# Kernel optimization log

Hardware: AMD Instinct MI355X
Metric: run time of the kernel (lower is better)

## Reference

```python
import jax, jax.numpy as jnp
import numpy as np

B, S, D, H = 2, 2048, 1024, 16
HD = D // H  # head_dim = 64
ROPE_BASE = 10000.0


def _rope_cos_sin(seq_len, head_dim, dtype):
    inv_freq = 1.0 / (ROPE_BASE ** (jnp.arange(0, head_dim, 2, dtype=jnp.float32) / head_dim))
    t = jnp.arange(seq_len, dtype=jnp.float32)
    freqs = jnp.einsum('i,j->ij', t, inv_freq)            # [S, HD/2]
    emb = jnp.concatenate([freqs, freqs], axis=-1)        # [S, HD]
    return jnp.cos(emb).astype(dtype), jnp.sin(emb).astype(dtype)


def _rotate_half(x):
    x1, x2 = jnp.split(x, 2, axis=-1)
    return jnp.concatenate([-x2, x1], axis=-1)


def setup_inputs() -> dict:
    key = jax.random.key(0)
    ks = jax.random.split(key, 5)
    scale = 1.0 / np.sqrt(D)
    x = jax.random.normal(ks[0], (B, S, D), dtype=jnp.float32)
    wq = jax.random.normal(ks[1], (D, D), dtype=jnp.float32) * scale
    wk = jax.random.normal(ks[2], (D, D), dtype=jnp.float32) * scale
    wv = jax.random.normal(ks[3], (D, D), dtype=jnp.float32) * scale
    wo = jax.random.normal(ks[4], (D, D), dtype=jnp.float32) * scale
    # causal additive mask: 0 on/below diagonal, -1e9 above
    causal = jnp.triu(jnp.full((S, S), -1e9, dtype=jnp.float32), k=1)
    attention_mask = causal[None, None, :, :]
    return {'x': x, 'attention_mask': attention_mask, 'wq': wq, 'wk': wk, 'wv': wv, 'wo': wo}


def reference(x, attention_mask, wq, wk, wv, wo):
    b, s, d = x.shape
    scale = 1.0 / np.sqrt(HD)
    # projections (torch Linear: y = x @ W.T)
    q = (x @ wq.T).reshape(b, s, H, HD).transpose(0, 2, 1, 3)  # [B,H,S,HD]
    k = (x @ wk.T).reshape(b, s, H, HD).transpose(0, 2, 1, 3)
    v = (x @ wv.T).reshape(b, s, H, HD).transpose(0, 2, 1, 3)
    cos, sin = _rope_cos_sin(s, HD, x.dtype)                   # [S, HD]
    cos = cos[None, None]
    sin = sin[None, None]
    q = q * cos + _rotate_half(q) * sin
    k = k * cos + _rotate_half(k) * sin
    scores = jnp.einsum('bhqd,bhkd->bhqk', q, k) * scale       # [B,H,S,S]
    scores = scores + attention_mask
    probs = jax.nn.softmax(scores, axis=-1)
    out = jnp.einsum('bhqk,bhkd->bhqd', probs, v)              # [B,H,S,HD]
    out = out.transpose(0, 2, 1, 3).reshape(b, s, d)
    return out @ wo.T
```

## Files before the change

kernel.cpp:

```cpp
#include <hip/hip_runtime.h>
#include <cstdint>
#include <cstddef>

typedef __attribute__((ext_vector_type(8))) _Float16 half8;
typedef __attribute__((ext_vector_type(4))) _Float16 half4;
typedef __attribute__((ext_vector_type(2))) __fp16 fp16x2;
typedef __attribute__((ext_vector_type(4))) float f32x4;

#define NB 2
#define NS 2048
#define ND 1024
#define NH 16
#define NHD 64
#define NM (NB * NS)

__device__ __forceinline__ void cvt8(const float* __restrict__ s,
                                     _Float16* __restrict__ d, int g) {
  const float4* s4 = (const float4*)s + (size_t)g * 2;
  float4 a = s4[0], b = s4[1];
  half8 h;
  h[0] = (_Float16)a.x; h[1] = (_Float16)a.y;
  h[2] = (_Float16)a.z; h[3] = (_Float16)a.w;
  h[4] = (_Float16)b.x; h[5] = (_Float16)b.y;
  h[6] = (_Float16)b.z; h[7] = (_Float16)b.w;
  *(half8*)(d + (size_t)g * 8) = h;
}

__global__ void prep(const float* __restrict__ x,
                     const float* __restrict__ wq, const float* __restrict__ wk,
                     const float* __restrict__ wv, const float* __restrict__ wo,
                     _Float16* __restrict__ xb,
                     _Float16* __restrict__ wqb, _Float16* __restrict__ wkb,
                     _Float16* __restrict__ wvb, _Float16* __restrict__ wob,
                     float* __restrict__ cosT, float* __restrict__ sinT) {
  int i = blockIdx.x * 256 + threadIdx.x;
  if (i < 524288) {
    cvt8(x, xb, i);
  } else if (i < 1048576) {
    int j = i - 524288;
    int k = j >> 17, g = j & 131071;
    const float* ws = (k == 0) ? wq : (k == 1) ? wk : (k == 2) ? wv : wo;
    _Float16* wd = (k == 0) ? wqb : (k == 1) ? wkb : (k == 2) ? wvb : wob;
    cvt8(ws, wd, g);
  } else if (i < 1056768) {
    int t0 = (i - 1048576) * 8;
#pragma unroll
    for (int e = 0; e < 8; ++e) {
      int t = t0 + e;
      int s = t >> 5, j = t & 31;
      float inv = expf(-(float)(2 * j) * (9.210340371976184f / 64.0f));
      float ang = (float)s * inv;
      cosT[t] = cosf(ang);
      sinT[t] = sinf(ang);
    }
  }
}

__device__ __forceinline__ void gload_lds16(const void* g, void* lds) {
  __builtin_amdgcn_global_load_lds(
      (const __attribute__((address_space(1))) unsigned int*)g,
      (__attribute__((address_space(3))) unsigned int*)lds, 16, 0, 0);
}

__device__ __forceinline__ float exp2_fast(float x) {
  float r;
  asm("v_exp_f32 %0, %1" : "=v"(r) : "v"(x));
  return r;
}

__device__ __forceinline__ void gemm_mainloop64(const _Float16* __restrict__ A,
                                                const _Float16* __restrict__ Bw,
                                                _Float16* As, _Float16* Bs,
                                                int brow, int bcol,
                                                int lane, int wid, int tid,
                                                f32x4 acc[4][4]) {
  const int l15 = lane & 15, l4 = lane >> 4;
  const int wr = wid >> 1, wc = wid & 1;
  const int rswz = (l15 & 7) << 4;
  const int srb = tid >> 3;
  const int scb = (tid & 7) * 16;

  for (int kt = 0; kt < ND / 64; ++kt) {
    const int k0 = kt * 64;
#pragma unroll
    for (int c = 0; c < 4; ++c) {
      const int r = c * 32 + srb;
      const int sb = scb ^ ((r & 7) << 4);
      gload_lds16((const char*)(A + (size_t)(brow + r) * ND + k0) + sb,
                  (char*)As + c * 4096 + tid * 16);
      gload_lds16((const char*)(Bw + (size_t)(bcol + r) * ND + k0) + sb,
                  (char*)Bs + c * 4096 + tid * 16);
    }
    __syncthreads();
#pragma unroll
    for (int kk = 0; kk < 2; ++kk) {
      half8 af[4], bf[4];
#pragma unroll
      for (int m = 0; m < 4; ++m) {
        const int row = wr * 64 + m * 16 + l15;
        af[m] = *(const half8*)((const char*)As +
                 ((row * 128 + kk * 64 + l4 * 16) ^ rswz));
      }
#pragma unroll
      for (int n = 0; n < 4; ++n) {
        const int row = wc * 64 + n * 16 + l15;
        bf[n] = *(const half8*)((const char*)Bs +
                 ((row * 128 + kk * 64 + l4 * 16) ^ rswz));
      }
#pragma unroll
      for (int m = 0; m < 4; ++m)
#pragma unroll
        for (int n = 0; n < 4; ++n)
          acc[m][n] = __builtin_amdgcn_mfma_f32_16x16x32_f16(af[m], bf[n],
                                                             acc[m][n], 0, 0, 0);
    }
    __syncthreads();
  }
}

__launch_bounds__(256, 2)
__global__ void qkv_gemm(const _Float16* __restrict__ X,
                         const _Float16* __restrict__ Wq,
                         const _Float16* __restrict__ Wk,
                         const _Float16* __restrict__ Wv,
                         _Float16* __restrict__ Qb,
                         _Float16* __restrict__ Kb,
                         _Float16* __restrict__ Vt,
                         const float* __restrict__ cosT,
                         const float* __restrict__ sinT) {
  __shared__ __align__(16) _Float16 As[128 * 64];
  __shared__ __align__(16) _Float16 Bs[128 * 64];
  const int tid = threadIdx.x, lane = tid & 63, wid = tid >> 6;
  const int l15 = lane & 15, l4 = lane >> 4;
  const int wr = wid >> 1, wc = wid & 1;
  const int brow = blockIdx.y * 128, bcol = blockIdx.x * 128;
  const int mode = blockIdx.z;
  const _Float16* W = (mode == 0) ? Wq : (mode == 1 ? Wk : Wv);

  f32x4 acc[4][4] = {};
  gemm_mainloop64(X, W, As, Bs, brow, bcol, lane, wid, tid, acc);

  const int b = brow >> 11;
  const int sbase = (brow & (NS - 1)) + wr * 64;
  const int h = (bcol >> 6) + wc;

  if (mode < 2) {
    _Float16* oh = ((mode == 0) ? Qb : Kb) + (size_t)(b * NH + h) * NS * NHD;
#pragma unroll
    for (int m = 0; m < 4; ++m) {
#pragma unroll
      for (int r = 0; r < 4; ++r) {
        const int s = sbase + m * 16 + l4 * 4 + r;
#pragma unroll
        for (int n = 0; n < 2; ++n) {
          const int hd = n * 16 + l15;
          const float c = cosT[s * 32 + hd];
          const float sn = sinT[s * 32 + hd];
          const float lo = acc[m][n][r], hi = acc[m][n + 2][r];
          oh[(size_t)s * NHD + hd]      = (_Float16)(lo * c - hi * sn);
          oh[(size_t)s * NHD + hd + 32] = (_Float16)(hi * c + lo * sn);
        }
      }
    }
  } else {
#pragma unroll
    for (int m = 0; m < 4; ++m) {
      const int s0 = sbase + m * 16 + l4 * 4;
      const int npos = (s0 & ~63) + (m >> 1) * 32 + l4 * 8 + (m & 1) * 4;
#pragma unroll
      for (int n = 0; n < 4; ++n) {
        const int hd = n * 16 + l15;
        half4 pk;
        pk[0] = (_Float16)acc[m][n][0];
        pk[1] = (_Float16)acc[m][n][1];
        pk[2] = (_Float16)acc[m][n][2];
        pk[3] = (_Float16)acc[m][n][3];
        *(half4*)(Vt + ((size_t)(b * NH + h) * NHD + hd) * NS + npos) = pk;
      }
    }
  }
}

__launch_bounds__(256, 4)
__global__ void flash_attn(const _Float16* __restrict__ Qb,
                           const _Float16* __restrict__ Kb,
                           const _Float16* __restrict__ Vt,
                           _Float16* __restrict__ Ob) {
  __shared__ __align__(16) _Float16 Ks[2][64 * 64];
  __shared__ __align__(16) _Float16 Vs[2][64 * 64];
  const int tid = threadIdx.x, lane = tid & 63, wid = tid >> 6;
  const int l15 = lane & 15, l4 = lane >> 4;
  const int bh = blockIdx.x & 31;
  const int qt = 31 - (blockIdx.x >> 5);
  const _Float16* Qh = Qb + (size_t)bh * NS * NHD;
  const char* Kg = (const char*)(Kb + (size_t)bh * NS * NHD);
  const char* Vg = (const char*)(Vt + (size_t)bh * NHD * NS);

  const float K1 = 0.125f * 1.4426950408889634f;
  const int swz_lane = ((lane >> 3) & 7) << 4;
  const int qloc = wid * 16 + l15;
  const int rswz = (l15 & 7) << 4;
  const int b = bh >> 4, h = bh & 15;
  const int nkt = qt + 1;

  half8 qf[2];
#pragma unroll
  for (int kk = 0; kk < 2; ++kk)
    qf[kk] = *(const half8*)&Qh[(size_t)(qt * 64 + wid * 16 + l15) * NHD + kk * 32 + l4 * 8];

  f32x4 oacc[4] = {};
  float mrun = -3.0e38f, lrun = 0.f;

#pragma unroll
  for (int c = 0; c < 2; ++c) {
    const int chunk = wid * 2 + c;
    const int slot = chunk * 1024 + lane * 16;
    const int sw = slot ^ swz_lane;
    gload_lds16(Kg + sw, (char*)&Ks[0][0] + slot);
    const int vrow = slot >> 7;
    gload_lds16(Vg + (size_t)vrow * (NS * 2) + (sw & 127), (char*)&Vs[0][0] + slot);
  }
  __syncthreads();

  int cur = 0;
  for (int kt = 0; kt < nkt; ++kt) {
    if (kt + 1 < nkt) {
      const size_t knext = (size_t)(kt + 1);
#pragma unroll
      for (int c = 0; c < 2; ++c) {
        const int chunk = wid * 2 + c;
        const int slot = chunk * 1024 + lane * 16;
        const int sw = slot ^ swz_lane;
        gload_lds16(Kg + knext * 8192 + sw, (char*)&Ks[cur ^ 1][0] + slot);
        const int vrow = slot >> 7;
        gload_lds16(Vg + (size_t)vrow * (NS * 2) + knext * 128 + (sw & 127),
                    (char*)&Vs[cur ^ 1][0] + slot);
      }
    }

    const bool diag = (kt == qt);
    const char* Kbuf = (const char*)&Ks[cur][0];
    const char* Vbuf = (const char*)&Vs[cur][0];

    f32x4 sacc[4] = {};
    __builtin_amdgcn_s_setprio(1);
#pragma unroll
    for (int kk = 0; kk < 2; ++kk) {
#pragma unroll
      for (int n = 0; n < 4; ++n) {
        if (diag && n > wid) continue;
        const int off = ((n * 16 + l15) * 128 + kk * 64 + l4 * 16) ^ rswz;
        half8 kf = *(const half8*)(Kbuf + off);
        sacc[n] = __builtin_amdgcn_mfma_f32_16x16x32_f16(kf, qf[kk], sacc[n], 0, 0, 0);
      }
    }
    __builtin_amdgcn_s_setprio(0);

    float traw[16];
#pragma unroll
    for (int n = 0; n < 4; ++n)
#pragma unroll
      for (int r = 0; r < 4; ++r) {
        float v = sacc[n][r];
        if (diag) {
          const int ki = n * 16 + l4 * 4 + r;
          v = (ki > qloc) ? -3.0e38f : v;
        }
        traw[n * 4 + r] = v;
      }
    float mx = traw[0];
#pragma unroll
    for (int j = 1; j < 16; ++j) mx = fmaxf(mx, traw[j]);
    mx = fmaxf(mx, __shfl_xor(mx, 16, 64));
    mx = fmaxf(mx, __shfl_xor(mx, 32, 64));
    mx *= K1;
    const float mnew = fmaxf(mrun, mx);
    const float alpha = exp2_fast(mrun - mnew);
    mrun = mnew;
    float ps[16], rs = 0.f;
#pragma unroll
    for (int j = 0; j < 16; ++j) {
      ps[j] = exp2_fast(__builtin_fmaf(traw[j], K1, -mnew));
      rs += ps[j];
    }
    rs += __shfl_xor(rs, 16, 64);
    rs += __shfl_xor(rs, 32, 64);
    lrun = lrun * alpha + rs;
#pragma unroll
    for (int n = 0; n < 4; ++n) oacc[n] *= alpha;

    __builtin_amdgcn_s_setprio(1);
#pragma unroll
    for (int c = 0; c < 2; ++c) {
      if (diag && c == 1 && wid < 2) continue;
      half8 pb;
#pragma unroll
      for (int q2 = 0; q2 < 4; ++q2) {
        fp16x2 pp = __builtin_amdgcn_cvt_pkrtz(ps[8 * c + 2 * q2],
                                               ps[8 * c + 2 * q2 + 1]);
        pb[2 * q2]     = (_Float16)pp[0];
        pb[2 * q2 + 1] = (_Float16)pp[1];
      }
#pragma unroll
      for (int n = 0; n < 4; ++n) {
        const int off = ((n * 16 + l15) * 128 + c * 64 + l4 * 16) ^ rswz;
        half8 va = *(const half8*)(Vbuf + off);
        oacc[n] = __builtin_amdgcn_mfma_f32_16x16x32_f16(va, pb, oacc[n], 0, 0, 0);
      }
    }
    __builtin_amdgcn_s_setprio(0);

    __syncthreads();
    cur ^= 1;
  }

  const int s = qt * 64 + wid * 16 + l15;
  const float invl = 1.0f / lrun;
#pragma unroll
  for (int n = 0; n < 4; ++n) {
    f32x4 ov = oacc[n] * invl;
    half4 o;
    o[0] = (_Float16)ov[0];
    o[1] = (_Float16)ov[1];
    o[2] = (_Float16)ov[2];
    o[3] = (_Float16)ov[3];
    *(half4*)&Ob[((size_t)(b * NS + s)) * ND + h * NHD + n * 16 + l4 * 4] = o;
  }
}

__launch_bounds__(256, 2)
__global__ void proj_gemm(const _Float16* __restrict__ A,
                          const _Float16* __restrict__ W,
                          float* __restrict__ out) {
  __shared__ __align__(16) _Float16 As[128 * 64];
  __shared__ __align__(16) _Float16 Bs[64 * 64];
  const int tid = threadIdx.x, lane = tid & 63, wid = tid >> 6;
  const int l15 = lane & 15, l4 = lane >> 4;
  const int wr = wid >> 1, wc = wid & 1;
  const int brow = blockIdx.y * 128, bcol = blockIdx.x * 64;
  const int rswz = (l15 & 7) << 4;
  const int srb = tid >> 3;
  const int scb = (tid & 7) * 16;

  f32x4 acc[4][2] = {};
  for (int kt = 0; kt < ND / 64; ++kt) {
    const int k0 = kt * 64;
#pragma unroll
    for (int c = 0; c < 4; ++c) {
      const int r = c * 32 + srb;
      const int sb = scb ^ ((r & 7) << 4);
      gload_lds16((const char*)(A + (size_t)(brow + r) * ND + k0) + sb,
                  (char*)As + c * 4096 + tid * 16);
    }
#pragma unroll
    for (int c = 0; c < 2; ++c) {
      const int r = c * 32 + srb;
      const int sb = scb ^ ((r & 7) << 4);
      gload_lds16((const char*)(W + (size_t)(bcol + r) * ND + k0) + sb,
                  (char*)Bs + c * 4096 + tid * 16);
    }
    __syncthreads();
#pragma unroll
    for (int kk = 0; kk < 2; ++kk) {
      half8 af[4], bf[2];
#pragma unroll
      for (int m = 0; m < 4; ++m) {
        const int row = wr * 64 + m * 16 + l15;
        af[m] = *(const half8*)((const char*)As +
                 ((row * 128 + kk * 64 + l4 * 16) ^ rswz));
      }
#pragma unroll
      for (int n = 0; n < 2; ++n) {
        const int row = wc * 32 + n * 16 + l15;
        bf[n] = *(const half8*)((const char*)Bs +
                 ((row * 128 + kk * 64 + l4 * 16) ^ rswz));
      }
#pragma unroll
      for (int m = 0; m < 4; ++m)
#pragma unroll
        for (int n = 0; n < 2; ++n)
          acc[m][n] = __builtin_amdgcn_mfma_f32_16x16x32_f16(af[m], bf[n],
                                                             acc[m][n], 0, 0, 0);
    }
    __syncthreads();
  }
#pragma unroll
  for (int m = 0; m < 4; ++m)
#pragma unroll
    for (int n = 0; n < 2; ++n)
#pragma unroll
      for (int r = 0; r < 4; ++r)
        out[(size_t)(brow + wr * 64 + m * 16 + l4 * 4 + r) * ND
            + bcol + wc * 32 + n * 16 + l15] = acc[m][n][r];
}

extern "C" void kernel_launch(void* const* d_in, const int* in_sizes, int n_in,
                              void* d_out, int out_size, void* d_ws, size_t ws_size,
                              hipStream_t stream) {
  const float* x  = (const float*)d_in[0];
  const float* wq = (const float*)d_in[2];
  const float* wk = (const float*)d_in[3];
  const float* wv = (const float*)d_in[4];
  const float* wo = (const float*)d_in[5];
  float* out = (float*)d_out;

  char* w = (char*)d_ws;
  _Float16* xb   = (_Float16*)(w);
  _Float16* wqb  = (_Float16*)(w + (8ull  << 20));
  _Float16* wkb  = (_Float16*)(w + (10ull << 20));
  _Float16* wvb  = (_Float16*)(w + (12ull << 20));
  _Float16* wob  = (_Float16*)(w + (14ull << 20));
  _Float16* Qb   = (_Float16*)(w + (16ull << 20));
  _Float16* Kb   = (_Float16*)(w + (24ull << 20));
  _Float16* Vt   = (_Float16*)(w + (32ull << 20));
  _Float16* Ob   = (_Float16*)(w + (40ull << 20));
  float*    cosT = (float*)   (w + (48ull << 20));
  float*    sinT = (float*)   (w + (48ull << 20) + (1ull << 18));

  dim3 blk(256);
  prep<<<4128, blk, 0, stream>>>(x, wq, wk, wv, wo, xb, wqb, wkb, wvb, wob,
                                 cosT, sinT);
  qkv_gemm<<<dim3(8, 32, 3), blk, 0, stream>>>(xb, wqb, wkb, wvb, Qb, Kb, Vt,
                                               cosT, sinT);
  flash_attn<<<1024, blk, 0, stream>>>(Qb, Kb, Vt, Ob);
  proj_gemm<<<dim3(16, 32), blk, 0, stream>>>(Ob, wob, out);
}
```

Before: 99.93 us.

## Split attention KV range across two blocks and merge with combine kernel

```diff
diff --git a/kernel.cpp b/kernel.cpp
--- a/kernel.cpp
+++ b/kernel.cpp
@@ -185,13 +185,21 @@
 __global__ void flash_attn(const _Float16* __restrict__ Qb,
                            const _Float16* __restrict__ Kb,
                            const _Float16* __restrict__ Vt,
-                           _Float16* __restrict__ Ob) {
+                           _Float16* __restrict__ Ob,
+                           _Float16* __restrict__ Op0,
+                           float2* __restrict__ ml) {
   __shared__ __align__(16) _Float16 Ks[2][64 * 64];
   __shared__ __align__(16) _Float16 Vs[2][64 * 64];
   const int tid = threadIdx.x, lane = tid & 63, wid = tid >> 6;
   const int l15 = lane & 15, l4 = lane >> 4;
   const int bh = blockIdx.x & 31;
-  const int qt = 31 - (blockIdx.x >> 5);
+  const int g = blockIdx.x >> 5;
+  const int qt = 31 - (g >> 1);
+  const int sp = 1 - (g & 1);
+  const int nkt = qt + 1;
+  const int hsp = nkt >> 1;
+  const int kt0 = sp ? hsp : 0;
+  const int ktend = sp ? nkt : hsp;
   const _Float16* Qh = Qb + (size_t)bh * NS * NHD;
   const char* Kg = (const char*)(Kb + (size_t)bh * NS * NHD);
   const char* Vg = (const char*)(Vt + (size_t)bh * NHD * NS);
@@ -201,7 +209,6 @@
   const int qloc = wid * 16 + l15;
   const int rswz = (l15 & 7) << 4;
   const int b = bh >> 4, h = bh & 15;
-  const int nkt = qt + 1;
 
   half8 qf[2];
 #pragma unroll
@@ -211,121 +218,168 @@
   f32x4 oacc[4] = {};
   float mrun = -3.0e38f, lrun = 0.f;
 
-#pragma unroll
-  for (int c = 0; c < 2; ++c) {
-    const int chunk = wid * 2 + c;
-    const int slot = chunk * 1024 + lane * 16;
-    const int sw = slot ^ swz_lane;
-    gload_lds16(Kg + sw, (char*)&Ks[0][0] + slot);
-    const int vrow = slot >> 7;
-    gload_lds16(Vg + (size_t)vrow * (NS * 2) + (sw & 127), (char*)&Vs[0][0] + slot);
-  }
-  __syncthreads();
-
-  int cur = 0;
-  for (int kt = 0; kt < nkt; ++kt) {
-    if (kt + 1 < nkt) {
-      const size_t knext = (size_t)(kt + 1);
+  if (kt0 < ktend) {
+#pragma unroll
+    for (int c = 0; c < 2; ++c) {
+      const int chunk = wid * 2 + c;
+      const int slot = chunk * 1024 + lane * 16;
+      const int sw = slot ^ swz_lane;
+      gload_lds16(Kg + (size_t)kt0 * 8192 + sw, (char*)&Ks[0][0] + slot);
+      const int vrow = slot >> 7;
+      gload_lds16(Vg + (size_t)vrow * (NS * 2) + kt0 * 128 + (sw & 127),
+                  (char*)&Vs[0][0] + slot);
+    }
+    __syncthreads();
+
+    int cur = 0;
+    for (int kt = kt0; kt < ktend; ++kt) {
+      if (kt + 1 < ktend) {
+        const size_t knext = (size_t)(kt + 1);
+#pragma unroll
+        for (int c = 0; c < 2; ++c) {
+          const int chunk = wid * 2 + c;
+          const int slot = chunk * 1024 + lane * 16;
+          const int sw = slot ^ swz_lane;
+          gload_lds16(Kg + knext * 8192 + sw, (char*)&Ks[cur ^ 1][0] + slot);
+          const int vrow = slot >> 7;
+          gload_lds16(Vg + (size_t)vrow * (NS * 2) + knext * 128 + (sw & 127),
+                      (char*)&Vs[cur ^ 1][0] + slot);
+        }
+      }
+
+      const bool diag = (kt == qt);
+      const char* Kbuf = (const char*)&Ks[cur][0];
+      const char* Vbuf = (const char*)&Vs[cur][0];
+
+      f32x4 sacc[4] = {};
+      __builtin_amdgcn_s_setprio(1);
+#pragma unroll
+      for (int kk = 0; kk < 2; ++kk) {
+#pragma unroll
+        for (int n = 0; n < 4; ++n) {
+          if (diag && n > wid) continue;
+          const int off = ((n * 16 + l15) * 128 + kk * 64 + l4 * 16) ^ rswz;
+          half8 kf = *(const half8*)(Kbuf + off);
+          sacc[n] = __builtin_amdgcn_mfma_f32_16x16x32_f16(kf, qf[kk], sacc[n], 0, 0, 0);
+        }
+      }
+      __builtin_amdgcn_s_setprio(0);
+
+      float traw[16];
+#pragma unroll
+      for (int n = 0; n < 4; ++n)
+#pragma unroll
+        for (int r = 0; r < 4; ++r) {
+          float v = sacc[n][r];
+          if (diag) {
+            const int ki = n * 16 + l4 * 4 + r;
+            v = (ki > qloc) ? -3.0e38f : v;
+          }
+          traw[n * 4 + r] = v;
+        }
+      float mx = traw[0];
+#pragma unroll
+      for (int j = 1; j < 16; ++j) mx = fmaxf(mx, traw[j]);
+      mx = fmaxf(mx, __shfl_xor(mx, 16, 64));
+      mx = fmaxf(mx, __shfl_xor(mx, 32, 64));
+      mx *= K1;
+      const float mnew = fmaxf(mrun, mx);
+      const float alpha = exp2_fast(mrun - mnew);
+      mrun = mnew;
+      float ps[16], rs = 0.f;
+#pragma unroll
+      for (int j = 0; j < 16; ++j) {
+        ps[j] = exp2_fast(__builtin_fmaf(traw[j], K1, -mnew));
+        rs += ps[j];
+      }
+      rs += __shfl_xor(rs, 16, 64);
+      rs += __shfl_xor(rs, 32, 64);
+      lrun = lrun * alpha + rs;
+#pragma unroll
+      for (int n = 0; n < 4; ++n) oacc[n] *= alpha;
+
+      __builtin_amdgcn_s_setprio(1);
 #pragma unroll
       for (int c = 0; c < 2; ++c) {
-        const int chunk = wid * 2 + c;
-        const int slot = chunk * 1024 + lane * 16;
-        const int sw = slot ^ swz_lane;
-        gload_lds16(Kg + knext * 8192 + sw, (char*)&Ks[cur ^ 1][0] + slot);
-        const int vrow = slot >> 7;
-        gload_lds16(Vg + (size_t)vrow * (NS * 2) + knext * 128 + (sw & 127),
-                    (char*)&Vs[cur ^ 1][0] + slot);
-      }
-    }
-
-    const bool diag = (kt == qt);
-    const char* Kbuf = (const char*)&Ks[cur][0];
-    const char* Vbuf = (const char*)&Vs[cur][0];
-
-    f32x4 sacc[4] = {};
-    __builtin_amdgcn_s_setprio(1);
-#pragma unroll
-    for (int kk = 0; kk < 2; ++kk) {
-#pragma unroll
-      for (int n = 0; n < 4; ++n) {
-        if (diag && n > wid) continue;
-        const int off = ((n * 16 + l15) * 128 + kk * 64 + l4 * 16) ^ rswz;
-        half8 kf = *(const half8*)(Kbuf + off);
-        sacc[n] = __builtin_amdgcn_mfma_f32_16x16x32_f16(kf, qf[kk], sacc[n], 0, 0, 0);
-      }
-    }
-    __builtin_amdgcn_s_setprio(0);
-
-    float traw[16];
-#pragma unroll
-    for (int n = 0; n < 4; ++n)
-#pragma unroll
-      for (int r = 0; r < 4; ++r) {
-        float v = sacc[n][r];
-        if (diag) {
-          const int ki = n * 16 + l4 * 4 + r;
-          v = (ki > qloc) ? -3.0e38f : v;
-        }
-        traw[n * 4 + r] = v;
-      }
-    float mx = traw[0];
-#pragma unroll
-    for (int j = 1; j < 16; ++j) mx = fmaxf(mx, traw[j]);
-    mx = fmaxf(mx, __shfl_xor(mx, 16, 64));
-    mx = fmaxf(mx, __shfl_xor(mx, 32, 64));
-    mx *= K1;
-    const float mnew = fmaxf(mrun, mx);
-    const float alpha = exp2_fast(mrun - mnew);
-    mrun = mnew;
-    float ps[16], rs = 0.f;
-#pragma unroll
-    for (int j = 0; j < 16; ++j) {
-      ps[j] = exp2_fast(__builtin_fmaf(traw[j], K1, -mnew));
-      rs += ps[j];
-    }
-    rs += __shfl_xor(rs, 16, 64);
-    rs += __shfl_xor(rs, 32, 64);
-    lrun = lrun * alpha + rs;
-#pragma unroll
-    for (int n = 0; n < 4; ++n) oacc[n] *= alpha;
-
-    __builtin_amdgcn_s_setprio(1);
-#pragma unroll
-    for (int c = 0; c < 2; ++c) {
-      if (diag && c == 1 && wid < 2) continue;
-      half8 pb;
-#pragma unroll
-      for (int q2 = 0; q2 < 4; ++q2) {
-        fp16x2 pp = __builtin_amdgcn_cvt_pkrtz(ps[8 * c + 2 * q2],
-                                               ps[8 * c + 2 * q2 + 1]);
-        pb[2 * q2]     = (_Float16)pp[0];
-        pb[2 * q2 + 1] = (_Float16)pp[1];
-      }
-#pragma unroll
-      for (int n = 0; n < 4; ++n) {
-        const int off = ((n * 16 + l15) * 128 + c * 64 + l4 * 16) ^ rswz;
-        half8 va = *(const half8*)(Vbuf + off);
-        oacc[n] = __builtin_amdgcn_mfma_f32_16x16x32_f16(va, pb, oacc[n], 0, 0, 0);
-      }
-    }
-    __builtin_amdgcn_s_setprio(0);
-
-    __syncthreads();
-    cur ^= 1;
-  }
-
-  const int s = qt * 64 + wid * 16 + l15;
-  const float invl = 1.0f / lrun;
-#pragma unroll
-  for (int n = 0; n < 4; ++n) {
-    f32x4 ov = oacc[n] * invl;
-    half4 o;
-    o[0] = (_Float16)ov[0];
-    o[1] = (_Float16)ov[1];
-    o[2] = (_Float16)ov[2];
-    o[3] = (_Float16)ov[3];
-    *(half4*)&Ob[((size_t)(b * NS + s)) * ND + h * NHD + n * 16 + l4 * 4] = o;
-  }
+        if (diag && c == 1 && wid < 2) continue;
+        half8 pb;
+#pragma unroll
+        for (int q2 = 0; q2 < 4; ++q2) {
+          fp16x2 pp = __builtin_amdgcn_cvt_pkrtz(ps[8 * c + 2 * q2],
+                                                 ps[8 * c + 2 * q2 + 1]);
+          pb[2 * q2]     = (_Float16)pp[0];
+          pb[2 * q2 + 1] = (_Float16)pp[1];
+        }
+#pragma unroll
+        for (int n = 0; n < 4; ++n) {
+          const int off = ((n * 16 + l15) * 128 + c * 64 + l4 * 16) ^ rswz;
+          half8 va = *(const half8*)(Vbuf + off);
+          oacc[n] = __builtin_amdgcn_mfma_f32_16x16x32_f16(va, pb, oacc[n], 0, 0, 0);
+        }
+      }
+      __builtin_amdgcn_s_setprio(0);
+
+      __syncthreads();
+      cur ^= 1;
+    }
+  }
+
+  const int q = qt * 64 + wid * 16 + l15;
+  const float invl = (lrun > 0.f) ? 1.0f / lrun : 0.f;
+  if (sp == 1) {
+#pragma unroll
+    for (int n = 0; n < 4; ++n) {
+      f32x4 ov = oacc[n] * invl;
+      half4 o;
+      o[0] = (_Float16)ov[0];
+      o[1] = (_Float16)ov[1];
+      o[2] = (_Float16)ov[2];
+      o[3] = (_Float16)ov[3];
+      *(half4*)&Ob[((size_t)(b * NS + q)) * ND + h * NHD + n * 16 + l4 * 4] = o;
+    }
+  } else {
+#pragma unroll
+    for (int n = 0; n < 4; ++n) {
+      f32x4 ov = oacc[n] * invl;
+      half4 o;
+      o[0] = (_Float16)ov[0];
+      o[1] = (_Float16)ov[1];
+      o[2] = (_Float16)ov[2];
+      o[3] = (_Float16)ov[3];
+      *(half4*)&Op0[((size_t)(bh * NS + q)) * NHD + n * 16 + l4 * 4] = o;
+    }
+  }
+  if (l4 == 0) {
+    float2 v;
+    v.x = mrun;
+    v.y = lrun;
+    ml[(size_t)sp * (32 * NS) + bh * NS + q] = v;
+  }
+}
+
+__global__ void combine(const _Float16* __restrict__ Op0,
+                        const float2* __restrict__ ml,
+                        _Float16* __restrict__ Ob) {
+  const int t = blockIdx.x * 256 + threadIdx.x;
+  const int r = t >> 3;
+  const int c = (t & 7) * 8;
+  const int bh = r >> 11, q = r & 2047;
+  const float2 a = ml[r];
+  const float2 bml = ml[32 * NS + r];
+  const float M = fmaxf(a.x, bml.x);
+  float w0 = exp2_fast(a.x - M) * a.y;
+  float w1 = exp2_fast(bml.x - M) * bml.y;
+  const float inv = 1.0f / (w0 + w1);
+  w0 *= inv; w1 *= inv;
+  const int b = bh >> 4, h = bh & 15;
+  const size_t obi = ((size_t)(b * NS + q)) * ND + h * NHD + c;
+  half8 o1 = *(const half8*)&Ob[obi];
+  half8 o0 = *(const half8*)&Op0[(size_t)r * NHD + c];
+  half8 o;
+#pragma unroll
+  for (int j = 0; j < 8; ++j)
+    o[j] = (_Float16)((float)o0[j] * w0 + (float)o1[j] * w1);
+  *(half8*)&Ob[obi] = o;
 }
 
 __launch_bounds__(256, 2)
@@ -416,12 +470,15 @@
   _Float16* Ob   = (_Float16*)(w + (40ull << 20));
   float*    cosT = (float*)   (w + (48ull << 20));
   float*    sinT = (float*)   (w + (48ull << 20) + (1ull << 18));
+  _Float16* Op0  = (_Float16*)(w);
+  float2*   ml   = (float2*)  (w + (10ull << 20));
 
   dim3 blk(256);
   prep<<<4128, blk, 0, stream>>>(x, wq, wk, wv, wo, xb, wqb, wkb, wvb, wob,
                                  cosT, sinT);
   qkv_gemm<<<dim3(8, 32, 3), blk, 0, stream>>>(xb, wqb, wkb, wvb, Qb, Kb, Vt,
                                                cosT, sinT);
-  flash_attn<<<1024, blk, 0, stream>>>(Qb, Kb, Vt, Ob);
+  flash_attn<<<2048, blk, 0, stream>>>(Qb, Kb, Vt, Ob, Op0, ml);
+  combine<<<2048, blk, 0, stream>>>(Op0, ml, Ob);
   proj_gemm<<<dim3(16, 32), blk, 0, stream>>>(Ob, wob, out);
 }
```

Measured after the change: 107.6 us. 7.6% more time.
